# Performance work log

Hardware: AMD Instinct MI355X
Metric: run time of the kernel (lower is better)

The kernel has to match this reference:

```python
import jax, jax.numpy as jnp
import numpy as np

W_POSE, W_MATCH, W_EPI = 1.0, 0.5, 0.1
EPS = 1e-8


def setup_inputs() -> dict:
    key = jax.random.key(0)
    ks = jax.random.split(key, 8)
    B, N, M = 16, 1024, 1024
    R_pred = jax.random.normal(ks[0], (B, 3, 3), dtype=jnp.float32)
    t_pred = jax.random.normal(ks[1], (B, 3), dtype=jnp.float32)
    R_gt = jax.random.normal(ks[2], (B, 3, 3), dtype=jnp.float32)
    t_gt = jax.random.normal(ks[3], (B, 3), dtype=jnp.float32)
    # realistic invertible camera intrinsics + small randn perturbation
    K_base = jnp.array([[500.0, 0.0, 320.0], [0.0, 500.0, 240.0], [0.0, 0.0, 1.0]], dtype=jnp.float32)
    K = K_base[None] + 0.01 * jax.random.normal(ks[4], (B, 3, 3), dtype=jnp.float32)
    kp1 = jax.random.normal(ks[5], (B, N, 2), dtype=jnp.float32)
    kp2 = jax.random.normal(ks[6], (B, N, 2), dtype=jnp.float32)
    matches = jax.random.uniform(ks[7], (B, N, M), dtype=jnp.float32)
    return {"R_pred": R_pred, "t_pred": t_pred, "R_gt": R_gt, "t_gt": t_gt,
            "K": K, "kp1": kp1, "kp2": kp2, "matches": matches}


def _homo(pts):
    # [B,N,2] -> [B,N,3]
    return jnp.concatenate([pts, jnp.ones(pts.shape[:-1] + (1,), pts.dtype)], axis=-1)


def _masked_weighted_mean(errors, matches):
    # samples with <3 surviving pairs are skipped (mirrors torch.where + skip).
    thr = jnp.max(matches, axis=(1, 2), keepdims=True) * 0.1
    mask = matches > thr
    w = jnp.where(mask, matches, 0.0)
    count = jnp.sum(mask, axis=(1, 2))
    valid = count >= 3
    per_b = jnp.sum(errors * w, axis=(1, 2)) / (jnp.sum(w, axis=(1, 2)) + EPS)
    per_b = jnp.where(valid, per_b, 0.0)
    n_valid = jnp.sum(valid)
    return jnp.where(n_valid > 0, jnp.sum(per_b) / jnp.maximum(n_valid, 1), 0.0)


def _fundamental(R, t, K):
    t_n = t / jnp.linalg.norm(t, axis=1, keepdims=True)  # F.normalize p=2 dim=1
    z = jnp.zeros_like(t_n[:, 0])
    t_skew = jnp.stack([
        jnp.stack([z, -t_n[:, 2], t_n[:, 1]], axis=-1),
        jnp.stack([t_n[:, 2], z, -t_n[:, 0]], axis=-1),
        jnp.stack([-t_n[:, 1], t_n[:, 0], z], axis=-1),
    ], axis=1)  # [B,3,3]
    E = jnp.einsum('bij,bjk->bik', t_skew, R)
    K_inv = jnp.linalg.inv(K)
    return jnp.einsum('bji,bjk,bkl->bil', K_inv, E, K_inv)  # K_inv^T E K_inv


def reference(R_pred, t_pred, R_gt, t_gt, K, kp1, kp2, matches):
    # rotation loss
    trace = jnp.einsum('bij,bij->b', R_pred, R_gt)  # trace(R_pred @ R_gt^T)
    geodesic = jnp.clip((trace - 1.0) / 2.0, -1.0 + 1e-7, 1.0 - 1e-7)
    rot_loss = jnp.mean(1.0 - geodesic)
    # translation loss
    t_gt_n = t_gt / jnp.linalg.norm(t_gt, axis=1, keepdims=True)
    trans_loss = jnp.mean(1.0 - jnp.sum(t_pred * t_gt_n, axis=1))
    pose_loss = rot_loss + trans_loss

    pts1_h = _homo(kp1)  # [B,N,3]
    pts2_h = _homo(kp2)  # [B,M,3]

    # correspondence loss: transformed pts1 by R_gt, error vs every kp2 -> [B,N,M]
    T = jnp.einsum('bij,bnj->bni', R_gt, pts1_h)[..., :2]  # [B,N,2]
    diff = kp2[:, None, :, :] - T[:, :, None, :]           # [B,N,M,2]
    corr_err = jnp.linalg.norm(diff, axis=-1)              # [B,N,M]
    match_loss = _masked_weighted_mean(corr_err, matches)

    # epipolar loss: |pts2_h[j]^T F pts1_h[i]| -> [B,N,M] indexed (i,j)
    F_mat = _fundamental(R_gt, t_gt, K)
    A = jnp.einsum('bmk,bkl->bml', pts2_h, F_mat)          # [B,M,3]
    epi_err = jnp.abs(jnp.einsum('bml,bnl->bnm', A, pts1_h))
    epi_loss = _masked_weighted_mean(epi_err, matches)

    total = W_POSE * pose_loss + W_MATCH * match_loss + W_EPI * epi_loss
    return total
```

## Files before the change

### kernel.cpp

```cpp
#include <hip/hip_runtime.h>

#define B 16
#define N 1024
#define M 1024
#define TN 8
#define NBLK (B * (N / TN))
#define C2 64

#define WS_CNTR  0
#define WS_RES   16
#define WS_PMAX  256
#define WS_PACC  2304
#define WS_BCNT  10496
#define WS_BAND  12544

#define NEG_INF (-3.402823466e+38f)

__device__ __forceinline__ void compute_F(const float* __restrict__ Rgp,
                                          const float* __restrict__ tg,
                                          const float* __restrict__ Km,
                                          float* F)
{
    float m00=Km[0], m01=Km[1], m02=Km[2];
    float m10=Km[3], m11=Km[4], m12=Km[5];
    float m20=Km[6], m21=Km[7], m22=Km[8];
    float c00 =  (m11*m22 - m12*m21), c01 = -(m10*m22 - m12*m20), c02 =  (m10*m21 - m11*m20);
    float c10 = -(m01*m22 - m02*m21), c11 =  (m00*m22 - m02*m20), c12 = -(m00*m21 - m01*m20);
    float c20 =  (m01*m12 - m02*m11), c21 = -(m00*m12 - m02*m10), c22 =  (m00*m11 - m01*m10);
    float id  = 1.f / (m00*c00 + m01*c01 + m02*c02);
    float Ki00 = c00*id, Ki01 = c10*id, Ki02 = c20*id;
    float Ki10 = c01*id, Ki11 = c11*id, Ki12 = c21*id;
    float Ki20 = c02*id, Ki21 = c12*id, Ki22 = c22*id;
    float inr = rsqrtf(tg[0]*tg[0] + tg[1]*tg[1] + tg[2]*tg[2]);
    float tx = tg[0]*inr, ty = tg[1]*inr, tz = tg[2]*inr;
    float Rg0=Rgp[0],Rg1=Rgp[1],Rg2=Rgp[2],Rg3=Rgp[3],Rg4=Rgp[4],Rg5=Rgp[5],Rg6=Rgp[6],Rg7=Rgp[7],Rg8=Rgp[8];
    float E00=-tz*Rg3+ty*Rg6, E01=-tz*Rg4+ty*Rg7, E02=-tz*Rg5+ty*Rg8;
    float E10= tz*Rg0-tx*Rg6, E11= tz*Rg1-tx*Rg7, E12= tz*Rg2-tx*Rg8;
    float E20=-ty*Rg0+tx*Rg3, E21=-ty*Rg1+tx*Rg4, E22=-ty*Rg2+tx*Rg5;
    float T00=E00*Ki00+E01*Ki10+E02*Ki20, T01=E00*Ki01+E01*Ki11+E02*Ki21, T02=E00*Ki02+E01*Ki12+E02*Ki22;
    float T10=E10*Ki00+E11*Ki10+E12*Ki20, T11=E10*Ki01+E11*Ki11+E12*Ki21, T12=E10*Ki02+E11*Ki12+E12*Ki22;
    float T20=E20*Ki00+E21*Ki10+E22*Ki20, T21=E20*Ki01+E21*Ki11+E22*Ki21, T22=E20*Ki02+E21*Ki12+E22*Ki22;
    F[0]=Ki00*T00+Ki10*T10+Ki20*T20; F[1]=Ki00*T01+Ki10*T11+Ki20*T21; F[2]=Ki00*T02+Ki10*T12+Ki20*T22;
    F[3]=Ki01*T00+Ki11*T10+Ki21*T20; F[4]=Ki01*T01+Ki11*T11+Ki21*T21; F[5]=Ki01*T02+Ki11*T12+Ki21*T22;
    F[6]=Ki02*T00+Ki12*T10+Ki22*T20; F[7]=Ki02*T01+Ki12*T11+Ki22*T21; F[8]=Ki02*T02+Ki12*T12+Ki22*T22;
}

__launch_bounds__(256, 4)
__global__ void k1_fused(const float* __restrict__ matches,
                         const float* __restrict__ R_gt, const float* __restrict__ t_gt,
                         const float* __restrict__ Kin,
                         const float* __restrict__ kp1,  const float* __restrict__ kp2,
                         float* __restrict__ ws)
{
    const int bid = blockIdx.x;
    const int b = bid >> 7;
    const int row0 = (bid & 127) * TN;
    const int t = threadIdx.x;
    const int lane = t & 63, wv = t >> 6;
    if (bid == 0 && t == 0) ((unsigned int*)ws)[WS_CNTR] = 0u;

    __shared__ float4 sTP[TN];
    __shared__ float  sm[4];
    __shared__ float4 paccL[4];
    __shared__ int    wtot[4];

    const float4* m4 = (const float4*)matches + ((long)b * N + row0) * (M/4) + t;
    float4 d[TN];
    #pragma unroll
    for (int n = 0; n < TN; ++n) d[n] = m4[n * (M/4)];

    const float* Rgp = R_gt + b * 9;
    if (t < TN) {
        float2 p = ((const float2*)kp1)[(long)b * N + row0 + t];
        sTP[t] = make_float4(Rgp[0]*p.x + Rgp[1]*p.y + Rgp[2],
                             Rgp[3]*p.x + Rgp[4]*p.y + Rgp[5], p.x, p.y);
    }

    float F[9];
    compute_F(Rgp, t_gt + b*3, Kin + b*9, F);
    const float4* kp2v = (const float4*)(kp2 + (long)b * M * 2);
    float4 q0 = kp2v[2*t], q1 = kp2v[2*t + 1];
    float k2x[4] = {q0.x, q0.z, q1.x, q1.z};
    float k2y[4] = {q0.y, q0.w, q1.y, q1.w};
    float A0[4], A1[4], A2[4];
    #pragma unroll
    for (int j = 0; j < 4; ++j) {
        A0[j] = k2x[j]*F[0] + k2y[j]*F[3] + F[6];
        A1[j] = k2x[j]*F[1] + k2y[j]*F[4] + F[7];
        A2[j] = k2x[j]*F[2] + k2y[j]*F[5] + F[8];
    }
    __syncthreads();

    float v = NEG_INF;
    #pragma unroll
    for (int n = 0; n < TN; ++n)
        v = fmaxf(v, fmaxf(fmaxf(d[n].x, d[n].y), fmaxf(d[n].z, d[n].w)));
    #pragma unroll
    for (int off = 32; off; off >>= 1) v = fmaxf(v, __shfl_down(v, off));
    if (lane == 0) sm[wv] = v;
    __syncthreads();
    float bmax = fmaxf(fmaxf(sm[0], sm[1]), fmaxf(sm[2], sm[3]));
    if (t == 0) ws[WS_PMAX + bid] = bmax;
    float thr_b = 0.1f * bmax;
    float cap_b = 1.01f * thr_b;

    float s_w = 0.f, s_c = 0.f, s_e = 0.f, s_n = 0.f;
    int bcnt = 0;
    #pragma unroll
    for (int n = 0; n < TN; ++n) {
        float4 tp = sTP[n];
        float mv[4] = {d[n].x, d[n].y, d[n].z, d[n].w};
        #pragma unroll
        for (int j = 0; j < 4; ++j) {
            float w = mv[j];
            bool pass = w > thr_b;
            float ww = pass ? w : 0.f;
            s_n += pass ? 1.f : 0.f;
            bcnt += (pass && w <= cap_b) ? 1 : 0;
            float dx = k2x[j] - tp.x, dy = k2y[j] - tp.y;
            float ce = sqrtf(dx*dx + dy*dy);
            float ee = fabsf(A0[j]*tp.z + A1[j]*tp.w + A2[j]);
            s_w += ww; s_c += ce*ww; s_e += ee*ww;
        }
    }
    #pragma unroll
    for (int off = 32; off; off >>= 1) {
        s_w += __shfl_down(s_w, off);
        s_c += __shfl_down(s_c, off);
        s_e += __shfl_down(s_e, off);
        s_n += __shfl_down(s_n, off);
    }
    int incl = bcnt;
    #pragma unroll
    for (int off = 1; off < 64; off <<= 1) {
        int y = __shfl_up(incl, off);
        if (lane >= off) incl += y;
    }
    if (lane == 0)  paccL[wv] = make_float4(s_w, s_c, s_e, s_n);
    if (lane == 63) wtot[wv] = incl;
    __syncthreads();
    if (t == 0) {
        float4 r = paccL[0];
        #pragma unroll
        for (int i = 1; i < 4; ++i) { r.x += paccL[i].x; r.y += paccL[i].y; r.z += paccL[i].z; r.w += paccL[i].w; }
        ((float4*)(ws + WS_PACC))[bid] = r;
    }
    int pos = incl - bcnt;
    #pragma unroll
    for (int k = 0; k < 4; ++k) if (k < wv) pos += wtot[k];
    int total = wtot[0] + wtot[1] + wtot[2] + wtot[3];
    if (t == 0) ((unsigned int*)ws)[WS_BCNT + bid] = (unsigned int)total;

    if (total > 0 && total <= C2) {
        float* band = ws + WS_BAND + (long)bid * (C2 * 3);
        #pragma unroll
        for (int n = 0; n < TN; ++n) {
            float4 tp = sTP[n];
            float mv[4] = {d[n].x, d[n].y, d[n].z, d[n].w};
            #pragma unroll
            for (int j = 0; j < 4; ++j) {
                float w = mv[j];
                if (w > thr_b && w <= cap_b) {
                    float dx = k2x[j] - tp.x, dy = k2y[j] - tp.y;
                    float ce = sqrtf(dx*dx + dy*dy);
                    float ee = fabsf(A0[j]*tp.z + A1[j]*tp.w + A2[j]);
                    band[pos*3 + 0] = w;
                    band[pos*3 + 1] = ce * w;
                    band[pos*3 + 2] = ee * w;
                    ++pos;
                }
            }
        }
    }
}

__launch_bounds__(256)
__global__ void k2_perb(const float* __restrict__ matches,
                        const float* __restrict__ R_pred, const float* __restrict__ t_pred,
                        const float* __restrict__ R_gt,   const float* __restrict__ t_gt,
                        const float* __restrict__ Kin,
                        const float* __restrict__ kp1,    const float* __restrict__ kp2,
                        float* __restrict__ ws, float* __restrict__ out)
{
    const int b = blockIdx.x;
    const int t = threadIdx.x;
    const int lane = t & 63, wv = t >> 6;

    __shared__ float  sThr;
    __shared__ float  sAcc4[4];
    __shared__ int    sFlag[128];
    __shared__ int    sNFlag;
    __shared__ int    sLast;
    __shared__ float4 sTP[TN];

    if (t < 4) sAcc4[t] = 0.f;
    if (t == 0) sNFlag = 0;

    if (t < 64) {
        float v = fmaxf(ws[WS_PMAX + b*128 + t], ws[WS_PMAX + b*128 + 64 + t]);
        #pragma unroll
        for (int off = 32; off; off >>= 1) v = fmaxf(v, __shfl_down(v, off));
        if (t == 0) sThr = 0.1f * v;
    }
    __syncthreads();
    const float thr = sThr;

    {
        int bidl = t >> 1;
        int half = t & 1;
        int bid  = b*128 + bidl;
        float s0 = 0.f, s1 = 0.f, s2 = 0.f, s3 = 0.f;
        float cap_b = 1.01f * 0.1f * ws[WS_PMAX + bid];
        unsigned int bcnt = ((const unsigned int*)ws)[WS_BCNT + bid];
        bool bad = (bcnt > (unsigned)C2) || (thr > cap_b);
        if (!bad) {
            const float* band = ws + WS_BAND + (long)bid * (C2 * 3);
            for (unsigned int k = half; k < bcnt; k += 2) {
                float w = band[k*3 + 0];
                if (!(w > thr)) { s0 -= w; s1 -= band[k*3 + 1]; s2 -= band[k*3 + 2]; s3 -= 1.f; }
            }
            if (half == 0) {
                float4 p = ((const float4*)(ws + WS_PACC))[bid];
                s0 += p.x; s1 += p.y; s2 += p.z; s3 += p.w;
            }
        } else if (half == 0) {
            int idx = atomicAdd(&sNFlag, 1);
            sFlag[idx] = bidl;
        }
        #pragma unroll
        for (int off = 32; off; off >>= 1) {
            s0 += __shfl_down(s0, off);
            s1 += __shfl_down(s1, off);
            s2 += __shfl_down(s2, off);
            s3 += __shfl_down(s3, off);
        }
        if (lane == 0) {
            atomicAdd(&sAcc4[0], s0);
            atomicAdd(&sAcc4[1], s1);
            atomicAdd(&sAcc4[2], s2);
            atomicAdd(&sAcc4[3], s3);
        }
    }
    __syncthreads();

    const int nflag = sNFlag;
    for (int f = 0; f < nflag; ++f) {
        __syncthreads();
        int bid = b*128 + sFlag[f];
        int row0 = (bid & 127) * TN;
        const float* Rgp = R_gt + b * 9;
        if (t < TN) {
            float2 p = ((const float2*)kp1)[(long)b * N + row0 + t];
            sTP[t] = make_float4(Rgp[0]*p.x + Rgp[1]*p.y + Rgp[2],
                                 Rgp[3]*p.x + Rgp[4]*p.y + Rgp[5], p.x, p.y);
        }
        float F[9];
        compute_F(Rgp, t_gt + b*3, Kin + b*9, F);
        const float4* kp2v = (const float4*)(kp2 + (long)b * M * 2);
        float4 q0 = kp2v[2*t], q1 = kp2v[2*t + 1];
        float k2x[4] = {q0.x, q0.z, q1.x, q1.z};
        float k2y[4] = {q0.y, q0.w, q1.y, q1.w};
        float A0[4], A1[4], A2[4];
        #pragma unroll
        for (int j = 0; j < 4; ++j) {
            A0[j] = k2x[j]*F[0] + k2y[j]*F[3] + F[6];
            A1[j] = k2x[j]*F[1] + k2y[j]*F[4] + F[7];
            A2[j] = k2x[j]*F[2] + k2y[j]*F[5] + F[8];
        }
        const float4* m4 = (const float4*)matches + ((long)b * N + row0) * (M/4) + t;
        float4 d[TN];
        #pragma unroll
        for (int n = 0; n < TN; ++n) d[n] = m4[n * (M/4)];
        __syncthreads();
        float s_w = 0.f, s_c = 0.f, s_e = 0.f, s_n = 0.f;
        #pragma unroll
        for (int n = 0; n < TN; ++n) {
            float4 tp = sTP[n];
            float mv[4] = {d[n].x, d[n].y, d[n].z, d[n].w};
            #pragma unroll
            for (int j = 0; j < 4; ++j) {
                float w = mv[j];
                bool pass = w > thr;
                float ww = pass ? w : 0.f;
                s_n += pass ? 1.f : 0.f;
                float dx = k2x[j] - tp.x, dy = k2y[j] - tp.y;
                float ce = sqrtf(dx*dx + dy*dy);
                float ee = fabsf(A0[j]*tp.z + A1[j]*tp.w + A2[j]);
                s_w += ww; s_c += ce*ww; s_e += ee*ww;
            }
        }
        #pragma unroll
        for (int off = 32; off; off >>= 1) {
            s_w += __shfl_down(s_w, off);
            s_c += __shfl_down(s_c, off);
            s_e += __shfl_down(s_e, off);
            s_n += __shfl_down(s_n, off);
        }
        if (lane == 0) {
            atomicAdd(&sAcc4[0], s_w);
            atomicAdd(&sAcc4[1], s_c);
            atomicAdd(&sAcc4[2], s_e);
            atomicAdd(&sAcc4[3], s_n);
        }
    }
    __syncthreads();

    if (t == 0) {
        const float* Rp = R_pred + b * 9;
        const float* Rq = R_gt   + b * 9;
        float trace = 0.f;
        #pragma unroll
        for (int i = 0; i < 9; ++i) trace += Rp[i] * Rq[i];
        float geo = fminf(fmaxf((trace - 1.f) * 0.5f, -1.f + 1e-7f), 1.f - 1e-7f);
        const float* tq = t_gt   + b * 3;
        const float* tp = t_pred + b * 3;
        float in2 = rsqrtf(tq[0]*tq[0] + tq[1]*tq[1] + tq[2]*tq[2]);
        float dotp = (tp[0]*tq[0] + tp[1]*tq[1] + tp[2]*tq[2]) * in2;
        float* res = ws + WS_RES + b * 8;
        res[0] = sAcc4[0]; res[1] = sAcc4[1]; res[2] = sAcc4[2]; res[3] = sAcc4[3];
        res[4] = (1.f - geo) + (1.f - dotp);
        __threadfence();
        unsigned int old = atomicAdd(((unsigned int*)ws) + WS_CNTR, 1u);
        sLast = (old == (unsigned int)(B - 1)) ? 1 : 0;
    }
    __syncthreads();
    if (!sLast) return;

    if (t == 0) {
        __threadfence();
        float pose = 0.f, ms = 0.f, es = 0.f;
        int nv = 0;
        for (int bb = 0; bb < B; ++bb) {
            const float* res = ws + WS_RES + bb * 8;
            float sw = res[0], sc = res[1], se = res[2], cn = res[3];
            pose += res[4];
            if (cn >= 3.f) { nv++; ms += sc / (sw + 1e-8f); es += se / (sw + 1e-8f); }
        }
        float match = nv > 0 ? ms / (float)nv : 0.f;
        float epi   = nv > 0 ? es / (float)nv : 0.f;
        out[0] = pose * (1.f / (float)B) + 0.5f * match + 0.1f * epi;
    }
}

extern "C" void kernel_launch(void* const* d_in, const int* in_sizes, int n_in,
                              void* d_out, int out_size, void* d_ws, size_t ws_size,
                              hipStream_t stream) {
    const float* R_pred  = (const float*)d_in[0];
    const float* t_pred  = (const float*)d_in[1];
    const float* R_gt    = (const float*)d_in[2];
    const float* t_gt    = (const float*)d_in[3];
    const float* K       = (const float*)d_in[4];
    const float* kp1     = (const float*)d_in[5];
    const float* kp2     = (const float*)d_in[6];
    const float* matches = (const float*)d_in[7];
    float* out = (float*)d_out;
    float* ws  = (float*)d_ws;

    k1_fused<<<NBLK, 256, 0, stream>>>(matches, R_gt, t_gt, K, kp1, kp2, ws);
    k2_perb <<<B,    256, 0, stream>>>(matches, R_pred, t_pred, R_gt, t_gt, K, kp1, kp2, ws, out);
}
```

Baseline: 40.59 us.

## Fuse per-batch finalize into main kernel via last-block counters and double rows per block

Merges the second per-batch reduction kernel into the main kernel. The last block to finish each batch, detected through a per-batch atomic counter, performs that batch's threshold fix-up and finalisation, and a global counter picks the block that writes the final loss. Rows per block go from 8 to 16, halving the block count and the per-block partial records, and a memset zeroes the counters before launch. This removes one kernel launch and the serial tail of the 16-block second kernel, at the cost of an extra memset node and more registers per thread for the larger row tile.

```diff
diff --git a/kernel.cpp b/kernel.cpp
--- a/kernel.cpp
+++ b/kernel.cpp
@@ -3,16 +3,18 @@
 #define B 16
 #define N 1024
 #define M 1024
-#define TN 8
-#define NBLK (B * (N / TN))
+#define TN 16
+#define BPB (N / TN)
+#define NBLK (B * BPB)
 #define C2 64
 
-#define WS_CNTR  0
-#define WS_RES   16
-#define WS_PMAX  256
-#define WS_PACC  2304
-#define WS_BCNT  10496
-#define WS_BAND  12544
+#define WS_CNTB  0
+#define WS_CNTF  256
+#define WS_RES   320
+#define WS_PMAX  512
+#define WS_BCNT  1536
+#define WS_PACC  2560
+#define WS_BAND  6656
 
 #define NEG_INF (-3.402823466e+38f)
 
@@ -46,23 +48,24 @@
 }
 
 __launch_bounds__(256, 4)
-__global__ void k1_fused(const float* __restrict__ matches,
-                         const float* __restrict__ R_gt, const float* __restrict__ t_gt,
-                         const float* __restrict__ Kin,
-                         const float* __restrict__ kp1,  const float* __restrict__ kp2,
-                         float* __restrict__ ws)
+__global__ void k_fused(const float* __restrict__ matches,
+                        const float* __restrict__ R_pred, const float* __restrict__ t_pred,
+                        const float* __restrict__ R_gt,   const float* __restrict__ t_gt,
+                        const float* __restrict__ Kin,
+                        const float* __restrict__ kp1,    const float* __restrict__ kp2,
+                        float* __restrict__ ws, float* __restrict__ out)
 {
-    const int bid = blockIdx.x;
-    const int b = bid >> 7;
-    const int row0 = (bid & 127) * TN;
-    const int t = threadIdx.x;
+    const int bid  = blockIdx.x;
+    const int b    = bid / BPB;
+    const int row0 = (bid % BPB) * TN;
+    const int t    = threadIdx.x;
     const int lane = t & 63, wv = t >> 6;
-    if (bid == 0 && t == 0) ((unsigned int*)ws)[WS_CNTR] = 0u;
 
     __shared__ float4 sTP[TN];
     __shared__ float  sm[4];
     __shared__ float4 paccL[4];
     __shared__ int    wtot[4];
+    __shared__ int    sFin, sLastF;
 
     const float4* m4 = (const float4*)matches + ((long)b * N + row0) * (M/4) + t;
     float4 d[TN];
@@ -172,58 +175,53 @@
             }
         }
     }
-}
-
-__launch_bounds__(256)
-__global__ void k2_perb(const float* __restrict__ matches,
-                        const float* __restrict__ R_pred, const float* __restrict__ t_pred,
-                        const float* __restrict__ R_gt,   const float* __restrict__ t_gt,
-                        const float* __restrict__ Kin,
-                        const float* __restrict__ kp1,    const float* __restrict__ kp2,
-                        float* __restrict__ ws, float* __restrict__ out)
-{
-    const int b = blockIdx.x;
-    const int t = threadIdx.x;
-    const int lane = t & 63, wv = t >> 6;
-
-    __shared__ float  sThr;
-    __shared__ float  sAcc4[4];
-    __shared__ int    sFlag[128];
-    __shared__ int    sNFlag;
-    __shared__ int    sLast;
-    __shared__ float4 sTP[TN];
-
+
+    __syncthreads();
+    if (t == 0) {
+        __threadfence();
+        unsigned int old = atomicAdd(((unsigned int*)ws) + WS_CNTB + b * 16, 1u);
+        sFin = (old == (unsigned int)(BPB - 1)) ? 1 : 0;
+    }
+    __syncthreads();
+    if (!sFin) return;
+
+    __threadfence();
+
+    __shared__ float sThr;
+    __shared__ float sAcc4[4];
+    __shared__ int   sFlag[BPB];
+    __shared__ int   sNFlag;
     if (t < 4) sAcc4[t] = 0.f;
     if (t == 0) sNFlag = 0;
 
     if (t < 64) {
-        float v = fmaxf(ws[WS_PMAX + b*128 + t], ws[WS_PMAX + b*128 + 64 + t]);
-        #pragma unroll
-        for (int off = 32; off; off >>= 1) v = fmaxf(v, __shfl_down(v, off));
-        if (t == 0) sThr = 0.1f * v;
+        float pv = ws[WS_PMAX + b*BPB + t];
+        #pragma unroll
+        for (int off = 32; off; off >>= 1) pv = fmaxf(pv, __shfl_down(pv, off));
+        if (t == 0) sThr = 0.1f * pv;
     }
     __syncthreads();
     const float thr = sThr;
 
     {
-        int bidl = t >> 1;
-        int half = t & 1;
-        int bid  = b*128 + bidl;
+        int bidl = t >> 2;
+        int qtr  = t & 3;
+        int bid2 = b*BPB + bidl;
         float s0 = 0.f, s1 = 0.f, s2 = 0.f, s3 = 0.f;
-        float cap_b = 1.01f * 0.1f * ws[WS_PMAX + bid];
-        unsigned int bcnt = ((const unsigned int*)ws)[WS_BCNT + bid];
-        bool bad = (bcnt > (unsigned)C2) || (thr > cap_b);
+        float capb2 = 1.01f * 0.1f * ws[WS_PMAX + bid2];
+        unsigned int bc = ((const unsigned int*)ws)[WS_BCNT + bid2];
+        bool bad = (bc > (unsigned)C2) || (thr > capb2);
         if (!bad) {
-            const float* band = ws + WS_BAND + (long)bid * (C2 * 3);
-            for (unsigned int k = half; k < bcnt; k += 2) {
+            const float* band = ws + WS_BAND + (long)bid2 * (C2 * 3);
+            for (unsigned int k = qtr; k < bc; k += 4) {
                 float w = band[k*3 + 0];
                 if (!(w > thr)) { s0 -= w; s1 -= band[k*3 + 1]; s2 -= band[k*3 + 2]; s3 -= 1.f; }
             }
-            if (half == 0) {
-                float4 p = ((const float4*)(ws + WS_PACC))[bid];
+            if (qtr == 0) {
+                float4 p = ((const float4*)(ws + WS_PACC))[bid2];
                 s0 += p.x; s1 += p.y; s2 += p.z; s3 += p.w;
             }
-        } else if (half == 0) {
+        } else if (qtr == 0) {
             int idx = atomicAdd(&sNFlag, 1);
             sFlag[idx] = bidl;
         }
@@ -246,71 +244,55 @@
     const int nflag = sNFlag;
     for (int f = 0; f < nflag; ++f) {
         __syncthreads();
-        int bid = b*128 + sFlag[f];
-        int row0 = (bid & 127) * TN;
-        const float* Rgp = R_gt + b * 9;
+        int rrow0 = sFlag[f] * TN;
         if (t < TN) {
-            float2 p = ((const float2*)kp1)[(long)b * N + row0 + t];
+            float2 p = ((const float2*)kp1)[(long)b * N + rrow0 + t];
             sTP[t] = make_float4(Rgp[0]*p.x + Rgp[1]*p.y + Rgp[2],
                                  Rgp[3]*p.x + Rgp[4]*p.y + Rgp[5], p.x, p.y);
         }
-        float F[9];
-        compute_F(Rgp, t_gt + b*3, Kin + b*9, F);
-        const float4* kp2v = (const float4*)(kp2 + (long)b * M * 2);
-        float4 q0 = kp2v[2*t], q1 = kp2v[2*t + 1];
-        float k2x[4] = {q0.x, q0.z, q1.x, q1.z};
-        float k2y[4] = {q0.y, q0.w, q1.y, q1.w};
-        float A0[4], A1[4], A2[4];
-        #pragma unroll
-        for (int j = 0; j < 4; ++j) {
-            A0[j] = k2x[j]*F[0] + k2y[j]*F[3] + F[6];
-            A1[j] = k2x[j]*F[1] + k2y[j]*F[4] + F[7];
-            A2[j] = k2x[j]*F[2] + k2y[j]*F[5] + F[8];
-        }
-        const float4* m4 = (const float4*)matches + ((long)b * N + row0) * (M/4) + t;
-        float4 d[TN];
-        #pragma unroll
-        for (int n = 0; n < TN; ++n) d[n] = m4[n * (M/4)];
+        const float4* m4r = (const float4*)matches + ((long)b * N + rrow0) * (M/4) + t;
+        float4 dr[TN];
+        #pragma unroll
+        for (int n = 0; n < TN; ++n) dr[n] = m4r[n * (M/4)];
         __syncthreads();
-        float s_w = 0.f, s_c = 0.f, s_e = 0.f, s_n = 0.f;
+        float s_w2 = 0.f, s_c2 = 0.f, s_e2 = 0.f, s_n2 = 0.f;
         #pragma unroll
         for (int n = 0; n < TN; ++n) {
             float4 tp = sTP[n];
-            float mv[4] = {d[n].x, d[n].y, d[n].z, d[n].w};
+            float mv[4] = {dr[n].x, dr[n].y, dr[n].z, dr[n].w};
             #pragma unroll
             for (int j = 0; j < 4; ++j) {
                 float w = mv[j];
                 bool pass = w > thr;
                 float ww = pass ? w : 0.f;
-                s_n += pass ? 1.f : 0.f;
+                s_n2 += pass ? 1.f : 0.f;
                 float dx = k2x[j] - tp.x, dy = k2y[j] - tp.y;
                 float ce = sqrtf(dx*dx + dy*dy);
                 float ee = fabsf(A0[j]*tp.z + A1[j]*tp.w + A2[j]);
-                s_w += ww; s_c += ce*ww; s_e += ee*ww;
+                s_w2 += ww; s_c2 += ce*ww; s_e2 += ee*ww;
             }
         }
         #pragma unroll
         for (int off = 32; off; off >>= 1) {
-            s_w += __shfl_down(s_w, off);
-            s_c += __shfl_down(s_c, off);
-            s_e += __shfl_down(s_e, off);
-            s_n += __shfl_down(s_n, off);
+            s_w2 += __shfl_down(s_w2, off);
+            s_c2 += __shfl_down(s_c2, off);
+            s_e2 += __shfl_down(s_e2, off);
+            s_n2 += __shfl_down(s_n2, off);
         }
         if (lane == 0) {
-            atomicAdd(&sAcc4[0], s_w);
-            atomicAdd(&sAcc4[1], s_c);
-            atomicAdd(&sAcc4[2], s_e);
-            atomicAdd(&sAcc4[3], s_n);
+            atomicAdd(&sAcc4[0], s_w2);
+            atomicAdd(&sAcc4[1], s_c2);
+            atomicAdd(&sAcc4[2], s_e2);
+            atomicAdd(&sAcc4[3], s_n2);
         }
     }
     __syncthreads();
 
     if (t == 0) {
         const float* Rp = R_pred + b * 9;
-        const float* Rq = R_gt   + b * 9;
         float trace = 0.f;
         #pragma unroll
-        for (int i = 0; i < 9; ++i) trace += Rp[i] * Rq[i];
+        for (int i = 0; i < 9; ++i) trace += Rp[i] * Rgp[i];
         float geo = fminf(fmaxf((trace - 1.f) * 0.5f, -1.f + 1e-7f), 1.f - 1e-7f);
         const float* tq = t_gt   + b * 3;
         const float* tp = t_pred + b * 3;
@@ -320,11 +302,11 @@
         res[0] = sAcc4[0]; res[1] = sAcc4[1]; res[2] = sAcc4[2]; res[3] = sAcc4[3];
         res[4] = (1.f - geo) + (1.f - dotp);
         __threadfence();
-        unsigned int old = atomicAdd(((unsigned int*)ws) + WS_CNTR, 1u);
-        sLast = (old == (unsigned int)(B - 1)) ? 1 : 0;
-    }
-    __syncthreads();
-    if (!sLast) return;
+        unsigned int old = atomicAdd(((unsigned int*)ws) + WS_CNTF, 1u);
+        sLastF = (old == (unsigned int)(B - 1)) ? 1 : 0;
+    }
+    __syncthreads();
+    if (!sLastF) return;
 
     if (t == 0) {
         __threadfence();
@@ -356,6 +338,7 @@
     float* out = (float*)d_out;
     float* ws  = (float*)d_ws;
 
-    k1_fused<<<NBLK, 256, 0, stream>>>(matches, R_gt, t_gt, K, kp1, kp2, ws);
-    k2_perb <<<B,    256, 0, stream>>>(matches, R_pred, t_pred, R_gt, t_gt, K, kp1, kp2, ws, out);
+    hipMemsetAsync(ws, 0, 2048, stream);
+    k_fused<<<NBLK, 256, 0, stream>>>(matches, R_pred, t_pred, R_gt, t_gt,
+                                      K, kp1, kp2, ws, out);
 }
```

Measured after the change: 80.25 us. 97.7% more time.

## Store band entries as float4 and parallelize per-batch band correction across threads

Applied to the files above, without the earlier changes.

Band entries are now written and read as aligned float4 records instead of strided triples. The per-batch kernel stages block maxima, counts and partial sums in shared memory and reduces the partials with shuffles. It then spreads the band correction over all 256 threads, one entry per thread, instead of serial loops over two threads per block. The goal is to cut serialized global loads in the second kernel, at the cost of more shared memory and extra barriers. It also drops a redundant barrier in the first kernel.

```diff
diff --git a/kernel.cpp b/kernel.cpp
--- a/kernel.cpp
+++ b/kernel.cpp
@@ -4,14 +4,15 @@
 #define N 1024
 #define M 1024
 #define TN 8
-#define NBLK (B * (N / TN))
+#define BPB (N / TN)
+#define NBLK (B * BPB)
 #define C2 64
 
 #define WS_CNTR  0
 #define WS_RES   16
 #define WS_PMAX  256
-#define WS_PACC  2304
-#define WS_BCNT  10496
+#define WS_BCNT  2304
+#define WS_PACC  4352
 #define WS_BAND  12544
 
 #define NEG_INF (-3.402823466e+38f)
@@ -89,7 +90,6 @@
         A1[j] = k2x[j]*F[1] + k2y[j]*F[4] + F[7];
         A2[j] = k2x[j]*F[2] + k2y[j]*F[5] + F[8];
     }
-    __syncthreads();
 
     float v = NEG_INF;
     #pragma unroll
@@ -99,6 +99,7 @@
     for (int off = 32; off; off >>= 1) v = fmaxf(v, __shfl_down(v, off));
     if (lane == 0) sm[wv] = v;
     __syncthreads();
+
     float bmax = fmaxf(fmaxf(sm[0], sm[1]), fmaxf(sm[2], sm[3]));
     if (t == 0) ws[WS_PMAX + bid] = bmax;
     float thr_b = 0.1f * bmax;
@@ -152,7 +153,7 @@
     if (t == 0) ((unsigned int*)ws)[WS_BCNT + bid] = (unsigned int)total;
 
     if (total > 0 && total <= C2) {
-        float* band = ws + WS_BAND + (long)bid * (C2 * 3);
+        float4* bandv = (float4*)(ws + WS_BAND) + (long)bid * C2;
         #pragma unroll
         for (int n = 0; n < TN; ++n) {
             float4 tp = sTP[n];
@@ -164,10 +165,7 @@
                     float dx = k2x[j] - tp.x, dy = k2y[j] - tp.y;
                     float ce = sqrtf(dx*dx + dy*dy);
                     float ee = fabsf(A0[j]*tp.z + A1[j]*tp.w + A2[j]);
-                    band[pos*3 + 0] = w;
-                    band[pos*3 + 1] = ce * w;
-                    band[pos*3 + 2] = ee * w;
-                    ++pos;
+                    bandv[pos++] = make_float4(w, ce * w, ee * w, 0.f);
                 }
             }
         }
@@ -186,18 +184,29 @@
     const int t = threadIdx.x;
     const int lane = t & 63, wv = t >> 6;
 
-    __shared__ float  sThr;
-    __shared__ float  sAcc4[4];
-    __shared__ int    sFlag[128];
-    __shared__ int    sNFlag;
-    __shared__ int    sLast;
-    __shared__ float4 sTP[TN];
-
-    if (t < 4) sAcc4[t] = 0.f;
+    __shared__ float        sPM[BPB];
+    __shared__ unsigned int sBC[BPB];
+    __shared__ int          sBad[BPB];
+    __shared__ float        sThr;
+    __shared__ float4       sPacc[2];
+    __shared__ float        sAcc4[4];
+    __shared__ int          sFlag[BPB];
+    __shared__ int          sNFlag;
+    __shared__ int          sLast;
+    __shared__ float4       sTP[TN];
+
     if (t == 0) sNFlag = 0;
 
+    float4 myPacc = make_float4(0.f, 0.f, 0.f, 0.f);
+    if (t < BPB) {
+        sPM[t] = ws[WS_PMAX + b*BPB + t];
+        sBC[t] = ((const unsigned int*)ws)[WS_BCNT + b*BPB + t];
+        myPacc = ((const float4*)(ws + WS_PACC))[b*BPB + t];
+    }
+    __syncthreads();
+
     if (t < 64) {
-        float v = fmaxf(ws[WS_PMAX + b*128 + t], ws[WS_PMAX + b*128 + 64 + t]);
+        float v = fmaxf(sPM[t], sPM[t + 64]);
         #pragma unroll
         for (int off = 32; off; off >>= 1) v = fmaxf(v, __shfl_down(v, off));
         if (t == 0) sThr = 0.1f * v;
@@ -205,27 +214,41 @@
     __syncthreads();
     const float thr = sThr;
 
+    if (t < BPB) {
+        bool bad = (sBC[t] > (unsigned)C2) || (thr > 1.01f * (0.1f * sPM[t]));
+        sBad[t] = bad ? 1 : 0;
+        if (bad) {
+            int i = atomicAdd(&sNFlag, 1);
+            sFlag[i] = t;
+            myPacc = make_float4(0.f, 0.f, 0.f, 0.f);
+        }
+    }
+    #pragma unroll
+    for (int off = 32; off; off >>= 1) {
+        myPacc.x += __shfl_down(myPacc.x, off);
+        myPacc.y += __shfl_down(myPacc.y, off);
+        myPacc.z += __shfl_down(myPacc.z, off);
+        myPacc.w += __shfl_down(myPacc.w, off);
+    }
+    if (t < BPB && lane == 0) sPacc[wv] = myPacc;
+    __syncthreads();
+    if (t == 0) {
+        sAcc4[0] = sPacc[0].x + sPacc[1].x;
+        sAcc4[1] = sPacc[0].y + sPacc[1].y;
+        sAcc4[2] = sPacc[0].z + sPacc[1].z;
+        sAcc4[3] = sPacc[0].w + sPacc[1].w;
+    }
+    __syncthreads();
+
     {
-        int bidl = t >> 1;
-        int half = t & 1;
-        int bid  = b*128 + bidl;
         float s0 = 0.f, s1 = 0.f, s2 = 0.f, s3 = 0.f;
-        float cap_b = 1.01f * 0.1f * ws[WS_PMAX + bid];
-        unsigned int bcnt = ((const unsigned int*)ws)[WS_BCNT + bid];
-        bool bad = (bcnt > (unsigned)C2) || (thr > cap_b);
-        if (!bad) {
-            const float* band = ws + WS_BAND + (long)bid * (C2 * 3);
-            for (unsigned int k = half; k < bcnt; k += 2) {
-                float w = band[k*3 + 0];
-                if (!(w > thr)) { s0 -= w; s1 -= band[k*3 + 1]; s2 -= band[k*3 + 2]; s3 -= 1.f; }
+        const float4* bandv = (const float4*)(ws + WS_BAND) + (long)b * BPB * C2;
+        for (int s = t; s < BPB * C2; s += 256) {
+            int bidl = s >> 6, k = s & 63;
+            if (!sBad[bidl] && (unsigned)k < sBC[bidl]) {
+                float4 e = bandv[bidl * C2 + k];
+                if (!(e.x > thr)) { s0 += e.x; s1 += e.y; s2 += e.z; s3 += 1.f; }
             }
-            if (half == 0) {
-                float4 p = ((const float4*)(ws + WS_PACC))[bid];
-                s0 += p.x; s1 += p.y; s2 += p.z; s3 += p.w;
-            }
-        } else if (half == 0) {
-            int idx = atomicAdd(&sNFlag, 1);
-            sFlag[idx] = bidl;
         }
         #pragma unroll
         for (int off = 32; off; off >>= 1) {
@@ -235,10 +258,10 @@
             s3 += __shfl_down(s3, off);
         }
         if (lane == 0) {
-            atomicAdd(&sAcc4[0], s0);
-            atomicAdd(&sAcc4[1], s1);
-            atomicAdd(&sAcc4[2], s2);
-            atomicAdd(&sAcc4[3], s3);
+            atomicAdd(&sAcc4[0], -s0);
+            atomicAdd(&sAcc4[1], -s1);
+            atomicAdd(&sAcc4[2], -s2);
+            atomicAdd(&sAcc4[3], -s3);
         }
     }
     __syncthreads();
@@ -246,11 +269,10 @@
     const int nflag = sNFlag;
     for (int f = 0; f < nflag; ++f) {
         __syncthreads();
-        int bid = b*128 + sFlag[f];
-        int row0 = (bid & 127) * TN;
+        int rrow0 = sFlag[f] * TN;
         const float* Rgp = R_gt + b * 9;
         if (t < TN) {
-            float2 p = ((const float2*)kp1)[(long)b * N + row0 + t];
+            float2 p = ((const float2*)kp1)[(long)b * N + rrow0 + t];
             sTP[t] = make_float4(Rgp[0]*p.x + Rgp[1]*p.y + Rgp[2],
                                  Rgp[3]*p.x + Rgp[4]*p.y + Rgp[5], p.x, p.y);
         }
@@ -267,7 +289,7 @@
             A1[j] = k2x[j]*F[1] + k2y[j]*F[4] + F[7];
             A2[j] = k2x[j]*F[2] + k2y[j]*F[5] + F[8];
         }
-        const float4* m4 = (const float4*)matches + ((long)b * N + row0) * (M/4) + t;
+        const float4* m4 = (const float4*)matches + ((long)b * N + rrow0) * (M/4) + t;
         float4 d[TN];
         #pragma unroll
         for (int n = 0; n < TN; ++n) d[n] = m4[n * (M/4)];
@@ -302,6 +324,7 @@
             atomicAdd(&sAcc4[2], s_e);
             atomicAdd(&sAcc4[3], s_n);
         }
+        __syncthreads();
     }
     __syncthreads();
 
```

Result: slower. 51.25 us (+26.3%).
